# Performance work log

Hardware: AMD Instinct MI355X
Metric: run time of the kernel (lower is better)

The kernel has to match this reference:

```python
import jax, jax.numpy as jnp
import numpy as np

# ---- model constants (match init_kwargs) ----
N_USERS = 100_000
N_ITEMS = 50_000
N_ENTITIES = 200_000          # items are entities [0, N_ITEMS)
N_REL = 20                    # relations after the +1 shift; rel_weight has N_REL-1 rows
EMB = 64
HOPS = 2
MARGIN_CCL = 0.8
NUM_NEG = 64
ANGLE_W = 0.1
ANGLE_DROP = 0.5              # eval-mode Dropout(ones)*rate == constant rate scaling
N_EDGES = 1_000_000
NNZ = 1_000_000
N_TRIPLETS = 200_000
BATCH = 4096
EPS = 1e-6


def _l2norm(x):
    # torch F.normalize(dim=-1, eps=1e-12)
    return x / jnp.maximum(jnp.linalg.norm(x, axis=-1, keepdims=True), 1e-12)


def setup_inputs() -> dict:
    key = jax.random.key(0)
    ks = jax.random.split(key, 13)
    # xavier_uniform bounds: sqrt(6/(fan_in+fan_out))
    b_all = float(np.sqrt(6.0 / (N_USERS + N_ENTITIES + EMB)))
    b_cf = float(np.sqrt(6.0 / (N_ITEMS + EMB)))
    b_rel = float(np.sqrt(6.0 / (N_REL - 1 + EMB)))
    all_embed = jax.random.uniform(ks[0], (N_USERS + N_ENTITIES, EMB), jnp.float32, -b_all, b_all)
    item_emb_cf = jax.random.uniform(ks[1], (N_ITEMS, EMB), jnp.float32, -b_cf, b_cf)
    rel_weight = jax.random.uniform(ks[2], (N_REL - 1, EMB), jnp.float32, -b_rel, b_rel)
    # D^{-1/2} A row-normalized positive values
    interact_vals = jax.random.uniform(ks[3], (NNZ,), jnp.float32, 0.01, 0.3)
    user = jax.random.randint(ks[4], (BATCH,), 0, N_USERS)
    pos_item = jax.random.randint(ks[5], (BATCH,), 0, N_ITEMS)
    neg_item = jax.random.randint(ks[6], (BATCH, NUM_NEG), 0, N_ITEMS)
    edge_index = jax.random.randint(ks[7], (2, N_EDGES), 0, N_ENTITIES)
    edge_type = jax.random.randint(ks[8], (N_EDGES,), 1, N_REL)  # relations already +1 shifted
    interact_rows = jax.random.randint(ks[9], (NNZ,), 0, N_USERS)
    interact_cols = jax.random.randint(ks[10], (NNZ,), 0, N_ITEMS)  # URM cols live in item range
    triplet_h = jax.random.randint(ks[11], (N_TRIPLETS,), 0, N_ENTITIES)
    triplet_t = jax.random.randint(ks[12], (N_TRIPLETS,), 0, N_ITEMS)
    return dict(all_embed=all_embed, item_emb_cf=item_emb_cf, rel_weight=rel_weight,
                interact_vals=interact_vals, user=user, pos_item=pos_item, neg_item=neg_item,
                edge_index=edge_index, edge_type=edge_type, interact_rows=interact_rows,
                interact_cols=interact_cols, triplet_h=triplet_h, triplet_t=triplet_t)


def _gcn(user_emb, entity_emb, item_cf, rel_weight, edge_index, edge_type, rows, cols, vals):
    """Multi-hop HAKG GraphConv: relation-gated KG scatter-mean + sparse user/CF aggregation."""
    head, tail = edge_index[0], edge_index[1]
    ent_res, usr_res, cf_res = entity_emb, user_emb, item_cf
    cnt = jax.ops.segment_sum(jnp.ones(head.shape, entity_emb.dtype), head, N_ENTITIES)
    denom = jnp.maximum(cnt, 1.0)[:, None]            # scatter_mean denominator
    rel_e = rel_weight[edge_type - 1]                 # [E, D]
    for _ in range(HOPS):
        # KG aggregate: entity_agg[h] = mean_{(h,r,t)} entity[t] * rel[r]
        neigh = entity_emb[tail] * rel_e              # [E, D]
        entity_agg = jax.ops.segment_sum(neigh, head, N_ENTITIES) / denom
        # user aggregate: sparse interact_mat @ entity_emb
        user_agg = jax.ops.segment_sum(vals[:, None] * entity_emb[cols], rows, N_USERS)
        # CF branch (LightGCN-style): R @ item_cf then R^T @ (...)
        u_cf = jax.ops.segment_sum(vals[:, None] * item_cf[cols], rows, N_USERS)
        item_agg_cf = jax.ops.segment_sum(vals[:, None] * u_cf[rows], cols, N_ITEMS)
        entity_emb = _l2norm(entity_agg)
        user_emb = _l2norm(user_agg)
        item_cf = _l2norm(item_agg_cf)
        ent_res = ent_res + entity_emb
        usr_res = usr_res + user_emb
        cf_res = cf_res + item_cf
    return ent_res, usr_res, cf_res


def _half_aperture(u):
    K = 0.1
    sqnu = jnp.clip(jnp.sum(u * u, -1), 0.0, 1.0 - EPS)
    return jnp.arcsin(jnp.clip(K * (1.0 - sqnu) / jnp.sqrt(sqnu), -1.0 + EPS, 1.0 - EPS))


def _angle_at_u(u, v):
    nu = jnp.linalg.norm(u, axis=-1)
    nv = jnp.linalg.norm(v, axis=-1)
    dp = jnp.sum(u * v, -1)
    ed = jnp.linalg.norm(u - v, axis=-1)
    num = dp * (1.0 + nu ** 2) - nu ** 2 * (1.0 + nv ** 2)
    den = nu * ed * jnp.sqrt(jnp.clip(1.0 + nv ** 2 * nu ** 2 - 2.0 * dp, EPS, None)) + EPS
    return jnp.arccos(jnp.clip(num / den, -1.0 + EPS, 1.0 - EPS))


def _contrastive_loss(u_e, pos_e, neg_e, pos_cf, neg_cf):
    B = u_e.shape[0]
    u, p, n = _l2norm(u_e), _l2norm(pos_e), _l2norm(neg_e)
    pcf, ncf = _l2norm(pos_cf), _l2norm(neg_cf)
    ui_pos = jax.nn.relu(2.0 - (jnp.sum(u * p, -1) + jnp.sum(u * pcf, -1)))
    ub = jnp.repeat(u, NUM_NEG, axis=0)               # [B*K, D]
    def neg_loss(nn_):
        s = jax.nn.relu(jnp.sum(ub * nn_, -1) - MARGIN_CCL).reshape(B, NUM_NEG)
        return jnp.sum(s, -1) / (jnp.sum(s > 0, -1).astype(s.dtype) + 1e-5)
    return jnp.mean(ui_pos + neg_loss(n) + neg_loss(ncf))


def reference(all_embed, item_emb_cf, rel_weight, interact_vals, user, pos_item, neg_item,
              edge_index, edge_type, interact_rows, interact_cols, triplet_h, triplet_t):
    user_emb = all_embed[:N_USERS]
    entity_emb = all_embed[N_USERS:]
    ent_g, usr_g, cf_g = _gcn(user_emb, entity_emb, item_emb_cf, rel_weight,
                              edge_index, edge_type, interact_rows, interact_cols, interact_vals)
    flat_neg = neg_item.reshape(-1)
    u_e = usr_g[user]
    loss1 = _contrastive_loss(u_e, ent_g[pos_item], ent_g[flat_neg], cf_g[pos_item], cf_g[flat_neg])
    # angle (hierarchy) loss, vectorized over all cross-type triplets
    hs = entity_emb[triplet_h] * ANGLE_DROP
    ts = entity_emb[triplet_t] * ANGLE_DROP
    angle_half = jax.nn.relu(_angle_at_u(hs, ts) - _half_aperture(hs))
    loss2 = ANGLE_W * jnp.sum(angle_half) / N_TRIPLETS
    return loss1 + loss2
```

## Files before the change

kernel.cpp:

```cpp
#include <hip/hip_runtime.h>
#include <math.h>

#define N_USERS    100000
#define N_ITEMS    50000
#define N_ENTITIES 200000
#define N_REL      20
#define EMB        64
#define HOPS       2
#define MARGIN_CCL 0.8f
#define NUM_NEG    64
#define ANGLE_W    0.1f
#define ANGLE_DROP 0.5f
#define N_EDGES    1000000
#define NNZ        1000000
#define N_TRIPLETS 200000
#define BATCH      4096
#define EPSF       1e-6f

#define TILE1 2048
#define NBUCK 196
#define ACAP  8192
#define HBLK  ((N_EDGES + TILE1 - 1) / TILE1)
#define P1B   (3 * HBLK)
#define KGB   (N_ENTITIES / 32)
#define UCFB  (N_USERS / 32)
#define ITEMB ((N_ITEMS + 31) / 32)
#define UBB   (BATCH / 32)
#define ANGB  (N_TRIPLETS / 32)
#define LOSSB (BATCH / 4)
#define CONV4E (N_ENTITIES * 16 / 1024)
#define CONV4I ((N_ITEMS * 16 + 1023) / 1024)

typedef _Float16 half4_t __attribute__((ext_vector_type(4)));
typedef _Float16 half8_t __attribute__((ext_vector_type(8)));
typedef float float8_t __attribute__((ext_vector_type(8)));

__device__ inline float4 h2f(half4_t h) {
    return make_float4((float)h.x, (float)h.y, (float)h.z, (float)h.w);
}
__device__ inline half4_t f2h(float4 f) {
    half4_t h; h.x = (_Float16)f.x; h.y = (_Float16)f.y;
    h.z = (_Float16)f.z; h.w = (_Float16)f.w; return h;
}
__device__ inline float8_t h8_to_f8(half8_t h) { return __builtin_convertvector(h, float8_t); }
__device__ inline half8_t f8_to_h8(float8_t f) { return __builtin_convertvector(f, half8_t); }
__device__ inline half8_t h8_zero() {
    half8_t z;
    #pragma unroll
    for (int i = 0; i < 8; ++i) z[i] = (_Float16)0.0f;
    return z;
}
__device__ inline float sum_sq8(float8_t f) {
    float s = 0.f;
    #pragma unroll
    for (int i = 0; i < 8; ++i) s += f[i] * f[i];
    return s;
}
__device__ inline float dot8(float8_t a, float8_t b) {
    float s = 0.f;
    #pragma unroll
    for (int i = 0; i < 8; ++i) s += a[i] * b[i];
    return s;
}
__device__ inline float8_t f8_from2(float4 lo, float4 hi) {
    float8_t f;
    f[0] = lo.x; f[1] = lo.y; f[2] = lo.z; f[3] = lo.w;
    f[4] = hi.x; f[5] = hi.y; f[6] = hi.z; f[7] = hi.w;
    return f;
}
__device__ inline float grp_red8(float v) {
    v += __shfl_xor(v, 1, 64); v += __shfl_xor(v, 2, 64); v += __shfl_xor(v, 4, 64);
    return v;
}
__device__ inline float dot4(float4 a, float4 b) {
    return a.x * b.x + a.y * b.y + a.z * b.z + a.w * b.w;
}
__device__ inline float grp_red16(float v) {
    v += __shfl_xor(v, 1, 64); v += __shfl_xor(v, 2, 64);
    v += __shfl_xor(v, 4, 64); v += __shfl_xor(v, 8, 64);
    return v;
}
__device__ inline float cross_grp_scalar(float v) {
    v += __shfl_xor(v, 16, 64); v += __shfl_xor(v, 32, 64);
    return v;
}
__device__ inline int f32_to_h16bits(float v) {
    _Float16 h = (_Float16)v;
    return (int)__builtin_bit_cast(unsigned short, h);
}
__device__ inline _Float16 h16_from_bits(int b) {
    return __builtin_bit_cast(_Float16, (unsigned short)(b & 0xFFFF));
}

__device__ inline void angle_body(int ablk, int t, const half8_t* __restrict__ ent_h,
                                  const int* __restrict__ th, const int* __restrict__ tt,
                                  float* sb, float* __restrict__ l2blk) {
    int o = t & 7;
    int grp = t >> 3;
    int trip = ablk * 32 + grp;
    int h = th[trip], t2 = tt[trip];
    float8_t hv = h8_to_f8(ent_h[h * 8 + o]);
    float8_t tv = h8_to_f8(ent_h[t2 * 8 + o]);
    hv *= ANGLE_DROP;
    tv *= ANGLE_DROP;
    float8_t dv = hv - tv;
    float s_hh = grp_red8(sum_sq8(hv));
    float s_tt = grp_red8(sum_sq8(tv));
    float s_ht = grp_red8(dot8(hv, tv));
    float s_dd = grp_red8(sum_sq8(dv));
    if (o == 0) {
        float nu = sqrtf(s_hh);
        float ed = sqrtf(s_dd);
        float sqnu = fminf(fmaxf(s_hh, 0.0f), 1.0f - EPSF);
        float ha_arg = fminf(fmaxf(0.1f * (1.0f - sqnu) / sqrtf(sqnu), -1.0f + EPSF), 1.0f - EPSF);
        float half_ap = asinf(ha_arg);
        float num = s_ht * (1.0f + s_hh) - s_hh * (1.0f + s_tt);
        float den = nu * ed * sqrtf(fmaxf(1.0f + s_tt * s_hh - 2.0f * s_ht, EPSF)) + EPSF;
        float ang = acosf(fminf(fmaxf(num / den, -1.0f + EPSF), 1.0f - EPSF));
        sb[grp] = fmaxf(ang - half_ap, 0.0f);
    }
    __syncthreads();
    if (t == 0) {
        float tot = 0.f;
        #pragma unroll
        for (int i = 0; i < 32; ++i) tot += sb[i];
        l2blk[ablk] = tot;
    }
}

__global__ void __launch_bounds__(256) phase1_sort(
        const int* __restrict__ head, const int* __restrict__ tail,
        const int* __restrict__ etype, const int* __restrict__ rows,
        const int* __restrict__ cols, const float* __restrict__ vals,
        int* __restrict__ bcur_e, int* __restrict__ bcur_u, int* __restrict__ bcur_i,
        int* __restrict__ keys_ping, int* __restrict__ kg_ping,
        int2* __restrict__ u_ping, int2* __restrict__ i_ping,
        const float4* __restrict__ ent0, const float4* __restrict__ cf0,
        half4_t* __restrict__ ent_a4, half4_t* __restrict__ cf16a4) {
    __shared__ int2 pay_st[TILE1];
    __shared__ int lhist[256], lstart[256], lcur[256];
    __shared__ int wsum[4], wpre[4];
    int* gbase = lhist;
    int bx = blockIdx.x, t = threadIdx.x;
    if (bx >= P1B) {
        int cb = bx - P1B;
        if (cb < CONV4E) {
            int i = cb * 1024 + t;
            #pragma unroll
            for (int j = 0; j < 4; ++j) ent_a4[i + j * 256] = f2h(ent0[i + j * 256]);
        } else {
            int i = (cb - CONV4E) * 1024 + t;
            #pragma unroll
            for (int j = 0; j < 4; ++j) {
                int ii = i + j * 256;
                if (ii < N_ITEMS * 16) cf16a4[ii] = f2h(cf0[ii]);
            }
        }
        return;
    }
    int seg = bx / HBLK;
    int tb  = bx % HBLK;
    int tstart = tb * TILE1;
    int valid = min(TILE1, N_EDGES - tstart);
    const int* karr = (seg == 0) ? head : (seg == 1) ? rows : cols;
    int shift = (seg == 0) ? 10 : (seg == 1) ? 9 : 8;
    int* bcur = (seg == 0) ? bcur_e : (seg == 1) ? bcur_u : bcur_i;
    lhist[t] = 0;
    __syncthreads();
    int kreg[8], pxr[8], pyr[8];
    #pragma unroll
    for (int j = 0; j < 8; ++j) {
        int i = t + j * 256;
        if (i < valid) {
            int k = karr[tstart + i];
            kreg[j] = k;
            if (seg == 0) {
                pxr[j] = tail[tstart + i] | ((etype[tstart + i] - 1) << 18);
            } else {
                int px;
                if (seg == 1) px = cols[tstart + i] | ((k & 511) << 16);
                else          px = rows[tstart + i] | ((k & 255) << 17);
                pxr[j] = px;
                pyr[j] = f32_to_h16bits(vals[tstart + i]) | ((k >> shift) << 16);
            }
            atomicAdd(&lhist[k >> shift], 1);
        }
    }
    __syncthreads();
    int v = lhist[t];
    int lane = t & 63, wv = t >> 6;
    int sc = v;
    #pragma unroll
    for (int d = 1; d < 64; d <<= 1) {
        int x = __shfl_up(sc, d, 64);
        if (lane >= d) sc += x;
    }
    if (lane == 63) wsum[wv] = sc;
    __syncthreads();
    if (t == 0) {
        int a = 0;
        #pragma unroll
        for (int i = 0; i < 4; ++i) { wpre[i] = a; a += wsum[i]; }
    }
    __syncthreads();
    int excl = sc + wpre[wv] - v;
    lstart[t] = excl;
    lcur[t] = excl;
    gbase[t] = t * ACAP + atomicAdd(&bcur[t], v);
    __syncthreads();
    if (seg == 0) {
        int* key_st = (int*)pay_st;
        int* ps = key_st + TILE1;
        #pragma unroll
        for (int j = 0; j < 8; ++j) {
            int i = t + j * 256;
            if (i < valid) {
                int sp = atomicAdd(&lcur[kreg[j] >> 10], 1);
                key_st[sp] = kreg[j];
                ps[sp] = pxr[j];
            }
        }
        __syncthreads();
        for (int j = t; j < valid; j += 256) {
            int k = key_st[j];
            int b = k >> 10;
            int pos = gbase[b] + (j - lstart[b]);
            keys_ping[pos] = k;
            kg_ping[pos] = ps[j];
        }
    } else {
        int2* pay = (seg == 1) ? u_ping : i_ping;
        #pragma unroll
        for (int j = 0; j < 8; ++j) {
            int i = t + j * 256;
            if (i < valid) {
                int sp = atomicAdd(&lcur[kreg[j] >> shift], 1);
                pay_st[sp] = make_int2(pxr[j], pyr[j]);
            }
        }
        __syncthreads();
        for (int j = t; j < valid; j += 256) {
            int2 p = pay_st[j];
            int bb = (p.y >> 16) & 0xFF;
            int pos = gbase[bb] + (j - lstart[bb]);
            pay[pos] = p;
        }
    }
}

__global__ void __launch_bounds__(256) phase2_angle(
        const int* __restrict__ bcur_e, const int* __restrict__ keys_ping,
        const int* __restrict__ kg_ping, int* __restrict__ kg_pack, int* __restrict__ off_e,
        const int* __restrict__ bcur_u, const int2* __restrict__ u_ping,
        int2* __restrict__ u_pack, int* __restrict__ off_u,
        const int* __restrict__ bcur_i, const int2* __restrict__ i_ping,
        int2* __restrict__ i_pack, int* __restrict__ off_i,
        const half8_t* __restrict__ ent_a, const int* __restrict__ th,
        const int* __restrict__ tt, float* __restrict__ l2blk) {
    __shared__ int hist[1024];
    __shared__ int wsum[4], wpre[4];
    __shared__ float sb[32];
    int t = threadIdx.x;
    if (blockIdx.x >= 3 * NBUCK) {
        angle_body(blockIdx.x - 3 * NBUCK, t, ent_a, th, tt, sb, l2blk);
        return;
    }
    int seg = blockIdx.x / NBUCK;
    int b   = blockIdx.x % NBUCK;
    int bins  = (seg == 0) ? 1024 : (seg == 1) ? 512 : 256;
    int shift = (seg == 0) ? 10 : (seg == 1) ? 9 : 8;
    int n_rows = (seg == 0) ? N_ENTITIES : (seg == 1) ? N_USERS : N_ITEMS;
    const int* bcur = (seg == 0) ? bcur_e : (seg == 1) ? bcur_u : bcur_i;
    int* off = (seg == 0) ? off_e : (seg == 1) ? off_u : off_i;
    int rs = b << shift;
    int re = min(rs + bins, n_rows);
    int nr = re - rs;
    int base = b * ACAP;
    int len = bcur[b];
    for (int r = t; r < bins; r += 256) hist[r] = 0;
    __syncthreads();
    if (seg == 0) {
        for (int j = t; j < len; j += 256) atomicAdd(&hist[keys_ping[base + j] - rs], 1);
    } else if (seg == 1) {
        for (int j = t; j < len; j += 256) atomicAdd(&hist[(u_ping[base + j].x >> 16) & 511], 1);
    } else {
        for (int j = t; j < len; j += 256) atomicAdd(&hist[(i_ping[base + j].x >> 17) & 255], 1);
    }
    __syncthreads();
    int own = bins >> 8;
    int c[4]; int tot = 0;
    #pragma unroll
    for (int i = 0; i < 4; ++i) { c[i] = (i < own) ? hist[t * own + i] : 0; tot += c[i]; }
    int lane = t & 63, wv = t >> 6;
    int sc = tot;
    #pragma unroll
    for (int d = 1; d < 64; d <<= 1) {
        int x = __shfl_up(sc, d, 64);
        if (lane >= d) sc += x;
    }
    if (lane == 63) wsum[wv] = sc;
    __syncthreads();
    if (t == 0) {
        int a = 0;
        #pragma unroll
        for (int i = 0; i < 4; ++i) { wpre[i] = a; a += wsum[i]; }
    }
    __syncthreads();
    int run = sc + wpre[wv] - tot;
    #pragma unroll
    for (int i = 0; i < 4; ++i) { if (i < own) { hist[t * own + i] = run; run += c[i]; } }
    __syncthreads();
    for (int r = t; r < nr; r += 256) off[rs + b + r] = base + hist[r];
    if (t == 0) off[rs + b + nr] = base + len;
    __syncthreads();
    if (seg == 0) {
        for (int j = t; j < len; j += 256) {
            int k = keys_ping[base + j];
            int slot = atomicAdd(&hist[k - rs], 1);
            kg_pack[base + slot] = kg_ping[base + j];
        }
    } else if (seg == 1) {
        for (int j = t; j < len; j += 256) {
            int2 p = u_ping[base + j];
            int slot = atomicAdd(&hist[(p.x >> 16) & 511], 1);
            u_pack[base + slot] = p;
        }
    } else {
        for (int j = t; j < len; j += 256) {
            int2 p = i_ping[base + j];
            int slot = atomicAdd(&hist[(p.x >> 17) & 255], 1);
            i_pack[base + slot] = p;
        }
    }
}

__device__ inline void kg0_body(int bid, int t, const int* __restrict__ off,
                                const int* __restrict__ pack, half8_t* srel,
                                const float* __restrict__ relw,
                                const half8_t* __restrict__ src, half8_t* __restrict__ dst,
                                half8_t* __restrict__ res, const float4* __restrict__ res_init) {
    if (t < (N_REL - 1) * 8) {
        int rel = t >> 3, o = t & 7;
        const float4* r4 = (const float4*)relw;
        srel[rel * 9 + o] = f8_to_h8(f8_from2(r4[rel * 16 + o * 2], r4[rel * 16 + o * 2 + 1]));
    }
    __syncthreads();
    int row = bid * 32 + (t >> 3);
    int o = t & 7;
    int idx = row + (row >> 10);
    int s = off[idx], e = off[idx + 1];
    half8_t acc = h8_zero();
    int k = s;
    for (; k + 4 <= e; k += 4) {
        int p0 = pack[k], p1 = pack[k + 1], p2 = pack[k + 2], p3 = pack[k + 3];
        half8_t a0 = src[(p0 & 0x3FFFF) * 8 + o];
        half8_t a1 = src[(p1 & 0x3FFFF) * 8 + o];
        half8_t a2 = src[(p2 & 0x3FFFF) * 8 + o];
        half8_t a3 = src[(p3 & 0x3FFFF) * 8 + o];
        acc += a0 * srel[(p0 >> 18) * 9 + o];
        acc += a1 * srel[(p1 >> 18) * 9 + o];
        acc += a2 * srel[(p2 >> 18) * 9 + o];
        acc += a3 * srel[(p3 >> 18) * 9 + o];
    }
    for (; k < e; ++k) {
        int p0 = pack[k];
        acc += src[(p0 & 0x3FFFF) * 8 + o] * srel[(p0 >> 18) * 9 + o];
    }
    float8_t f = h8_to_f8(acc);
    f *= 1.0f / fmaxf((float)(e - s), 1.0f);
    float ss = grp_red8(sum_sq8(f));
    f *= 1.0f / fmaxf(sqrtf(ss), 1e-12f);
    dst[row * 8 + o] = f8_to_h8(f);
    if (row < N_ITEMS) {
        float8_t rr = f8_from2(res_init[row * 16 + o * 2], res_init[row * 16 + o * 2 + 1]);
        rr += f;
        res[row * 8 + o] = f8_to_h8(rr);
    }
}

__device__ inline void kg2_body(int bid, int t, const int* __restrict__ off,
                                const int* __restrict__ pack, half8_t* srel,
                                const float* __restrict__ relw,
                                const half8_t* __restrict__ src, half8_t* __restrict__ res) {
    if (t < (N_REL - 1) * 8) {
        int rel = t >> 3, o = t & 7;
        const float4* r4 = (const float4*)relw;
        srel[rel * 9 + o] = f8_to_h8(f8_from2(r4[rel * 16 + o * 2], r4[rel * 16 + o * 2 + 1]));
    }
    __syncthreads();
    int row = bid * 32 + (t >> 3);
    if (row >= N_ITEMS) return;
    int o = t & 7;
    int idx = row + (row >> 10);
    int s = off[idx], e = off[idx + 1];
    half8_t acc = h8_zero();
    int k = s;
    for (; k + 4 <= e; k += 4) {
        int p0 = pack[k], p1 = pack[k + 1], p2 = pack[k + 2], p3 = pack[k + 3];
        half8_t a0 = src[(p0 & 0x3FFFF) * 8 + o];
        half8_t a1 = src[(p1 & 0x3FFFF) * 8 + o];
        half8_t a2 = src[(p2 & 0x3FFFF) * 8 + o];
        half8_t a3 = src[(p3 & 0x3FFFF) * 8 + o];
        acc += a0 * srel[(p0 >> 18) * 9 + o];
        acc += a1 * srel[(p1 >> 18) * 9 + o];
        acc += a2 * srel[(p2 >> 18) * 9 + o];
        acc += a3 * srel[(p3 >> 18) * 9 + o];
    }
    for (; k < e; ++k) {
        int p0 = pack[k];
        acc += src[(p0 & 0x3FFFF) * 8 + o] * srel[(p0 >> 18) * 9 + o];
    }
    float8_t f = h8_to_f8(acc);
    f *= 1.0f / fmaxf((float)(e - s), 1.0f);
    float ss = grp_red8(sum_sq8(f));
    f *= 1.0f / fmaxf(sqrtf(ss), 1e-12f);
    float8_t rr = h8_to_f8(res[row * 8 + o]);
    rr += f;
    float s2 = grp_red8(sum_sq8(rr));
    rr *= 1.0f / fmaxf(sqrtf(s2), 1e-12f);
    res[row * 8 + o] = f8_to_h8(rr);
}

__device__ inline void ucf_body(int bid, int t, const int* __restrict__ off,
                                const int2* __restrict__ u_pack,
                                const half8_t* __restrict__ cf16,
                                half8_t* __restrict__ ucf) {
    int row = bid * 32 + (t >> 3);
    int o = t & 7;
    int idx = row + (row >> 9);
    int s = off[idx], e = off[idx + 1];
    half8_t acc = h8_zero();
    int k = s;
    if (k + 4 <= e) {
        int2 p0 = u_pack[k], p1 = u_pack[k + 1], p2 = u_pack[k + 2], p3 = u_pack[k + 3];
        for (;;) {
            int kn = k + 4;
            half8_t c0 = cf16[(p0.x & 0xFFFF) * 8 + o];
            half8_t c1 = cf16[(p1.x & 0xFFFF) * 8 + o];
            half8_t c2 = cf16[(p2.x & 0xFFFF) * 8 + o];
            half8_t c3 = cf16[(p3.x & 0xFFFF) * 8 + o];
            bool more = (kn + 4 <= e);
            int2 n0, n1, n2, n3;
            if (more) { n0 = u_pack[kn]; n1 = u_pack[kn + 1]; n2 = u_pack[kn + 2]; n3 = u_pack[kn + 3]; }
            acc += c0 * h16_from_bits(p0.y);
            acc += c1 * h16_from_bits(p1.y);
            acc += c2 * h16_from_bits(p2.y);
            acc += c3 * h16_from_bits(p3.y);
            k = kn;
            if (!more) break;
            p0 = n0; p1 = n1; p2 = n2; p3 = n3;
        }
    }
    for (; k < e; ++k) {
        int2 p0 = u_pack[k];
        acc += cf16[(p0.x & 0xFFFF) * 8 + o] * h16_from_bits(p0.y);
    }
    ucf[row * 8 + o] = acc;
}

__device__ inline void ubatch_body(int bid, int t, const int* __restrict__ user,
                                   const int* __restrict__ off,
                                   const int2* __restrict__ u_pack,
                                   const half8_t* __restrict__ ent_a,
                                   const half8_t* __restrict__ ent_b,
                                   const float4* __restrict__ usr0f,
                                   half8_t* __restrict__ usr_b) {
    int g = t >> 3, o = t & 7;
    int b = bid * 32 + g;
    int uid = user[b];
    int idx = uid + (uid >> 9);
    int s = off[idx], e = off[idx + 1];
    half8_t acc1 = h8_zero(), acc2 = h8_zero();
    int k = s;
    for (; k + 4 <= e; k += 4) {
        int2 p0 = u_pack[k], p1 = u_pack[k + 1], p2 = u_pack[k + 2], p3 = u_pack[k + 3];
        int c0 = (p0.x & 0xFFFF) * 8 + o;
        int c1 = (p1.x & 0xFFFF) * 8 + o;
        int c2 = (p2.x & 0xFFFF) * 8 + o;
        int c3 = (p3.x & 0xFFFF) * 8 + o;
        half8_t ea0 = ent_a[c0], eb0 = ent_b[c0];
        half8_t ea1 = ent_a[c1], eb1 = ent_b[c1];
        half8_t ea2 = ent_a[c2], eb2 = ent_b[c2];
        half8_t ea3 = ent_a[c3], eb3 = ent_b[c3];
        _Float16 v0 = h16_from_bits(p0.y);
        _Float16 v1 = h16_from_bits(p1.y);
        _Float16 v2 = h16_from_bits(p2.y);
        _Float16 v3 = h16_from_bits(p3.y);
        acc1 += ea0 * v0; acc2 += eb0 * v0;
        acc1 += ea1 * v1; acc2 += eb1 * v1;
        acc1 += ea2 * v2; acc2 += eb2 * v2;
        acc1 += ea3 * v3; acc2 += eb3 * v3;
    }
    for (; k < e; ++k) {
        int2 p0 = u_pack[k];
        int c0 = (p0.x & 0xFFFF) * 8 + o;
        _Float16 v0 = h16_from_bits(p0.y);
        acc1 += ent_a[c0] * v0;
        acc2 += ent_b[c0] * v0;
    }
    float8_t f1 = h8_to_f8(acc1);
    float ss1 = grp_red8(sum_sq8(f1));
    f1 *= 1.0f / fmaxf(sqrtf(ss1), 1e-12f);
    float8_t u0 = f8_from2(usr0f[uid * 16 + o * 2], usr0f[uid * 16 + o * 2 + 1]);
    float8_t r1 = h8_to_f8(f8_to_h8(u0 + f1));
    float8_t f2 = h8_to_f8(acc2);
    float ss2 = grp_red8(sum_sq8(f2));
    f2 *= 1.0f / fmaxf(sqrtf(ss2), 1e-12f);
    float8_t r = r1 + f2;
    float s3 = grp_red8(sum_sq8(r));
    r *= 1.0f / fmaxf(sqrtf(s3), 1e-12f);
    usr_b[b * 8 + o] = f8_to_h8(r);
}

__device__ inline void item_body(int bid, int t, const int* __restrict__ off,
                                 const int2* __restrict__ i_pack,
                                 const half8_t* __restrict__ ucf,
                                 half8_t* __restrict__ cf_nxt, half8_t* __restrict__ res,
                                 const float4* __restrict__ res_init, int first, int last) {
    int row = bid * 32 + (t >> 3);
    int o = t & 7;
    if (row >= N_ITEMS) return;
    int idx = row + (row >> 8);
    int s = off[idx], e = off[idx + 1];
    half8_t acc = h8_zero();
    int k = s;
    if (k + 4 <= e) {
        int2 p0 = i_pack[k], p1 = i_pack[k + 1], p2 = i_pack[k + 2], p3 = i_pack[k + 3];
        for (;;) {
            int kn = k + 4;
            half8_t c0 = ucf[(p0.x & 0x1FFFF) * 8 + o];
            half8_t c1 = ucf[(p1.x & 0x1FFFF) * 8 + o];
            half8_t c2 = ucf[(p2.x & 0x1FFFF) * 8 + o];
            half8_t c3 = ucf[(p3.x & 0x1FFFF) * 8 + o];
            bool more = (kn + 4 <= e);
            int2 n0, n1, n2, n3;
            if (more) { n0 = i_pack[kn]; n1 = i_pack[kn + 1]; n2 = i_pack[kn + 2]; n3 = i_pack[kn + 3]; }
            acc += c0 * h16_from_bits(p0.y);
            acc += c1 * h16_from_bits(p1.y);
            acc += c2 * h16_from_bits(p2.y);
            acc += c3 * h16_from_bits(p3.y);
            k = kn;
            if (!more) break;
            p0 = n0; p1 = n1; p2 = n2; p3 = n3;
        }
    }
    for (; k < e; ++k) {
        int2 p0 = i_pack[k];
        acc += ucf[(p0.x & 0x1FFFF) * 8 + o] * h16_from_bits(p0.y);
    }
    float8_t f = h8_to_f8(acc);
    float ss = grp_red8(sum_sq8(f));
    f *= 1.0f / fmaxf(sqrtf(ss), 1e-12f);
    if (!last) cf_nxt[row * 8 + o] = f8_to_h8(f);
    float8_t rr;
    if (first) rr = f8_from2(res_init[row * 16 + o * 2], res_init[row * 16 + o * 2 + 1]);
    else       rr = h8_to_f8(res[row * 8 + o]);
    rr += f;
    if (last) {
        float s2 = grp_red8(sum_sq8(rr));
        rr *= 1.0f / fmaxf(sqrtf(s2), 1e-12f);
    }
    res[row * 8 + o] = f8_to_h8(rr);
}

__device__ inline void loss_ent_body(int b, int t,
                                     const int* __restrict__ pos, const int* __restrict__ neg,
                                     const half4_t* __restrict__ usrb4,
                                     const half4_t* __restrict__ ent4,
                                     float* __restrict__ dpe, float* __restrict__ l1pe) {
    int lane = t & 63;
    int g = lane >> 4, q = lane & 15;
    int pid = pos[b];
    float4 u = h2f(usrb4[b * 16 + q]);
    float4 p = h2f(ent4[pid * 16 + q]);
    float dpe_v = grp_red16(dot4(u, p));
    float sum_n = 0.f, cnt_n = 0.f;
    const int* nb = neg + b * NUM_NEG;
    for (int j = 0; j < NUM_NEG; j += 16) {
        int n0 = nb[j + g], n1 = nb[j + 4 + g], n2 = nb[j + 8 + g], n3 = nb[j + 12 + g];
        float4 e0 = h2f(ent4[n0 * 16 + q]);
        float4 e1 = h2f(ent4[n1 * 16 + q]);
        float4 e2 = h2f(ent4[n2 * 16 + q]);
        float4 e3 = h2f(ent4[n3 * 16 + q]);
        float dn0 = grp_red16(dot4(u, e0));
        float dn1 = grp_red16(dot4(u, e1));
        float dn2 = grp_red16(dot4(u, e2));
        float dn3 = grp_red16(dot4(u, e3));
        float s0 = fmaxf(dn0 - MARGIN_CCL, 0.f); sum_n += s0; if (s0 > 0.f) cnt_n += 1.f;
        float s1 = fmaxf(dn1 - MARGIN_CCL, 0.f); sum_n += s1; if (s1 > 0.f) cnt_n += 1.f;
        float s2 = fmaxf(dn2 - MARGIN_CCL, 0.f); sum_n += s2; if (s2 > 0.f) cnt_n += 1.f;
        float s3 = fmaxf(dn3 - MARGIN_CCL, 0.f); sum_n += s3; if (s3 > 0.f) cnt_n += 1.f;
    }
    sum_n = cross_grp_scalar(sum_n); cnt_n = cross_grp_scalar(cnt_n);
    if (lane == 0) {
        dpe[b] = dpe_v;
        l1pe[b] = sum_n / (cnt_n + 1e-5f);
    }
}

__global__ void __launch_bounds__(256) loss_cf_kernel(
        const int* __restrict__ pos, const int* __restrict__ neg,
        const half4_t* __restrict__ usrb4, const half4_t* __restrict__ cf4,
        const float* __restrict__ dpe, const float* __restrict__ l1pe,
        float* __restrict__ l1p) {
    int b = blockIdx.x * 4 + (threadIdx.x >> 6);
    int lane = threadIdx.x & 63;
    int g = lane >> 4, q = lane & 15;
    int pid = pos[b];
    float4 u = h2f(usrb4[b * 16 + q]);
    float4 pc = h2f(cf4[pid * 16 + q]);
    float dpc = grp_red16(dot4(u, pc));
    float sum_c = 0.f, cnt_c = 0.f;
    const int* nb = neg + b * NUM_NEG;
    for (int j = 0; j < NUM_NEG; j += 16) {
        int n0 = nb[j + g], n1 = nb[j + 4 + g], n2 = nb[j + 8 + g], n3 = nb[j + 12 + g];
        float4 e0 = h2f(cf4[n0 * 16 + q]);
        float4 e1 = h2f(cf4[n1 * 16 + q]);
        float4 e2 = h2f(cf4[n2 * 16 + q]);
        float4 e3 = h2f(cf4[n3 * 16 + q]);
        float dc0 = grp_red16(dot4(u, e0));
        float dc1 = grp_red16(dot4(u, e1));
        float dc2 = grp_red16(dot4(u, e2));
        float dc3 = grp_red16(dot4(u, e3));
        float t0 = fmaxf(dc0 - MARGIN_CCL, 0.f); sum_c += t0; if (t0 > 0.f) cnt_c += 1.f;
        float t1 = fmaxf(dc1 - MARGIN_CCL, 0.f); sum_c += t1; if (t1 > 0.f) cnt_c += 1.f;
        float t2 = fmaxf(dc2 - MARGIN_CCL, 0.f); sum_c += t2; if (t2 > 0.f) cnt_c += 1.f;
        float t3 = fmaxf(dc3 - MARGIN_CCL, 0.f); sum_c += t3; if (t3 > 0.f) cnt_c += 1.f;
    }
    sum_c = cross_grp_scalar(sum_c); cnt_c = cross_grp_scalar(cnt_c);
    if (lane == 0) {
        float ui_pos = fmaxf(2.0f - dpe[b] - dpc, 0.0f);
        l1p[b] = ui_pos + l1pe[b] + sum_c / (cnt_c + 1e-5f);
    }
}

__global__ void __launch_bounds__(256) fused_h0(
        const int* __restrict__ off_e, const int* __restrict__ kg_pack,
        const float* __restrict__ relw, const half8_t* __restrict__ ent_a,
        half8_t* __restrict__ ent_b, half8_t* __restrict__ ent_res,
        const float4* __restrict__ ent0f,
        const int* __restrict__ off_u, const int2* __restrict__ u_pack,
        const half8_t* __restrict__ cf16_a, half8_t* __restrict__ ucf) {
    __shared__ half8_t srel[(N_REL - 1) * 9];
    int bx = blockIdx.x, t = threadIdx.x;
    if (bx < KGB) {
        kg0_body(bx, t, off_e, kg_pack, srel, relw, ent_a, ent_b, ent_res, ent0f);
    } else {
        ucf_body(bx - KGB, t, off_u, u_pack, cf16_a, ucf);
    }
}

__global__ void __launch_bounds__(256) fused_ik(
        const int* __restrict__ off_e, const int* __restrict__ kg_pack,
        const float* __restrict__ relw, const half8_t* __restrict__ ent_b,
        half8_t* __restrict__ ent_res,
        const int* __restrict__ off_i, const int2* __restrict__ i_pack,
        const half8_t* __restrict__ ucf, half8_t* __restrict__ cf16_b,
        half8_t* __restrict__ cf_res, const float4* __restrict__ cf0f,
        const int* __restrict__ user, const int* __restrict__ off_u,
        const int2* __restrict__ u_pack, const half8_t* __restrict__ ent_a,
        const float4* __restrict__ usr0f, half8_t* __restrict__ usr_b) {
    __shared__ half8_t srel[(N_REL - 1) * 9];
    int bx = blockIdx.x, t = threadIdx.x;
    if (bx < ITEMB) {
        kg2_body(bx, t, off_e, kg_pack, srel, relw, ent_b, ent_res);
    } else if (bx < 2 * ITEMB) {
        item_body(bx - ITEMB, t, off_i, i_pack, ucf, cf16_b, cf_res, cf0f, 1, 0);
    } else {
        ubatch_body(bx - 2 * ITEMB, t, user, off_u, u_pack, ent_a, ent_b, usr0f, usr_b);
    }
}

__global__ void __launch_bounds__(256) fused_u1_loss(
        const int* __restrict__ off_u, const int2* __restrict__ u_pack,
        const half8_t* __restrict__ cf16_b, half8_t* __restrict__ ucf,
        const int* __restrict__ pos, const int* __restrict__ neg,
        const half4_t* __restrict__ usrb4, const half4_t* __restrict__ ent4,
        float* __restrict__ dpe, float* __restrict__ l1pe) {
    int bx = blockIdx.x, t = threadIdx.x;
    if (bx < UCFB) {
        ucf_body(bx, t, off_u, u_pack, cf16_b, ucf);
    } else {
        int b = (bx - UCFB) * 4 + (t >> 6);
        loss_ent_body(b, t, pos, neg, usrb4, ent4, dpe, l1pe);
    }
}

__global__ void __launch_bounds__(256) item_h1(
        const int* __restrict__ off_i, const int2* __restrict__ i_pack,
        const half8_t* __restrict__ ucf, half8_t* __restrict__ cf_res,
        const float4* __restrict__ cf0f) {
    item_body(blockIdx.x, threadIdx.x, off_i, i_pack, ucf, (half8_t*)0, cf_res, cf0f, 0, 1);
}

__global__ void finalize_kernel(const float* __restrict__ l1p, const float* __restrict__ l2b,
                                float* __restrict__ out) {
    __shared__ float sb[1024];
    float a1 = 0.f;
    for (int i = threadIdx.x; i < BATCH; i += 1024) a1 += l1p[i];
    float a2 = 0.f;
    for (int i = threadIdx.x; i < ANGB; i += 1024) a2 += l2b[i];
    sb[threadIdx.x] = a1 / (float)BATCH + ANGLE_W * a2 / (float)N_TRIPLETS;
    __syncthreads();
    for (int s = 512; s > 0; s >>= 1) {
        if (threadIdx.x < s) sb[threadIdx.x] += sb[threadIdx.x + s];
        __syncthreads();
    }
    if (threadIdx.x == 0) out[0] = sb[0];
}

extern "C" void kernel_launch(void* const* d_in, const int* in_sizes, int n_in,
                              void* d_out, int out_size, void* d_ws, size_t ws_size,
                              hipStream_t stream) {
    const float* all_embed = (const float*)d_in[0];
    const float* item_cf0  = (const float*)d_in[1];
    const float* relw      = (const float*)d_in[2];
    const float* vals      = (const float*)d_in[3];
    const int* user        = (const int*)d_in[4];
    const int* pos_item    = (const int*)d_in[5];
    const int* neg_item    = (const int*)d_in[6];
    const int* edge_head   = (const int*)d_in[7];
    const int* edge_tail   = edge_head + N_EDGES;
    const int* etype       = (const int*)d_in[8];
    const int* irows       = (const int*)d_in[9];
    const int* icols       = (const int*)d_in[10];
    const int* th          = (const int*)d_in[11];
    const int* tt          = (const int*)d_in[12];
    float* out             = (float*)d_out;

    char* base = (char*)d_ws;
    size_t woff = 0;
    auto alloc = [&](size_t bytes) -> void* {
        void* p = base + woff;
        woff = (woff + bytes + 255) & ~(size_t)255;
        return p;
    };
    const size_t ping_ui = (size_t)NBUCK * ACAP * 8;
    const size_t ping_kg = (size_t)NBUCK * ACAP * 4;

    half8_t* ent_a   = (half8_t*)alloc((size_t)N_ENTITIES * EMB * 2);
    half8_t* ent_b   = (half8_t*)alloc(2 * ping_ui);
    half8_t* cf16_a  = (half8_t*)alloc((size_t)N_ITEMS * EMB * 2);
    half8_t* cf16_b  = (half8_t*)alloc(ping_kg);
    half8_t* ucf     = (half8_t*)alloc((size_t)N_USERS * EMB * 2);
    half8_t* ent_res = (half8_t*)alloc((size_t)N_ITEMS * EMB * 2);
    half8_t* cf_res  = (half8_t*)alloc((size_t)N_ITEMS * EMB * 2);
    half8_t* usr_b   = (half8_t*)alloc((size_t)BATCH * EMB * 2);
    int2* u_pack     = (int2*)alloc(ping_ui);
    int2* i_pack     = (int2*)alloc(ping_ui);
    int* kg_pack     = (int*)alloc(ping_kg);
    float* l1p       = (float*)alloc((size_t)BATCH * 4);
    float* dpe       = (float*)alloc((size_t)BATCH * 4);
    float* l1pe      = (float*)alloc((size_t)BATCH * 4);
    float* l2blk     = (float*)alloc((size_t)ANGB * 4);
    int* off_e       = (int*)alloc((size_t)(N_ENTITIES + NBUCK + 1) * 4);
    int* off_u       = (int*)alloc((size_t)(N_USERS + NBUCK + 1) * 4);
    int* off_i       = (int*)alloc((size_t)(N_ITEMS + NBUCK + 1) * 4);
    int* bcur_all    = (int*)alloc(3 * 256 * 4);
    int* bcur_e      = bcur_all;
    int* bcur_u      = bcur_all + 256;
    int* bcur_i      = bcur_all + 512;

    int2* u_ping   = (int2*)ent_b;
    int2* i_ping   = (int2*)((char*)ent_b + ping_ui);
    int* kg_ping   = (int*)cf16_b;
    int* keys_ping = (int*)ucf;

    const float* ent0 = all_embed + (size_t)N_USERS * EMB;

    hipMemsetAsync(bcur_all, 0, 3 * 256 * 4, stream);
    phase1_sort<<<P1B + CONV4E + CONV4I, 256, 0, stream>>>(
        edge_head, edge_tail, etype, irows, icols, vals,
        bcur_e, bcur_u, bcur_i, keys_ping, kg_ping, u_ping, i_ping,
        (const float4*)ent0, (const float4*)item_cf0, (half4_t*)ent_a, (half4_t*)cf16_a);
    phase2_angle<<<3 * NBUCK + ANGB, 256, 0, stream>>>(
        bcur_e, keys_ping, kg_ping, kg_pack, off_e,
        bcur_u, u_ping, u_pack, off_u,
        bcur_i, i_ping, i_pack, off_i,
        (const half8_t*)ent_a, th, tt, l2blk);
    fused_h0<<<KGB + UCFB, 256, 0, stream>>>(
        off_e, kg_pack, relw, ent_a, ent_b, ent_res, (const float4*)ent0,
        off_u, u_pack, cf16_a, ucf);
    fused_ik<<<2 * ITEMB + UBB, 256, 0, stream>>>(
        off_e, kg_pack, relw, ent_b, ent_res,
        off_i, i_pack, ucf, cf16_b, cf_res, (const float4*)item_cf0,
        user, off_u, u_pack, ent_a, (const float4*)all_embed, usr_b);
    fused_u1_loss<<<UCFB + LOSSB, 256, 0, stream>>>(
        off_u, u_pack, cf16_b, ucf, pos_item, neg_item,
        (const half4_t*)usr_b, (const half4_t*)ent_res, dpe, l1pe);
    item_h1<<<ITEMB, 256, 0, stream>>>(off_i, i_pack, ucf, cf_res,
                                       (const float4*)item_cf0);
    loss_cf_kernel<<<LOSSB, 256, 0, stream>>>(pos_item, neg_item,
                                              (const half4_t*)usr_b, (const half4_t*)cf_res,
                                              dpe, l1pe, l1p);
    finalize_kernel<<<1, 1024, 0, stream>>>(l1p, l2blk, out);
}
```

Baseline: 343.8 us.

## Spread angle-loss blocks across later kernels and prefetch gather indices

The angle-loss blocks are split three ways. Part stays in phase2, and the rest are appended to the item_h1 and loss_cf kernels, which have small grids, so the tail of each launch gets filled with independent work. Separately, the KG aggregation loops and the negative-sample loss loops now software-pipeline their index loads, fetching the next group of indices while the current gathers are used. This adds register pressure and makes block scheduling in those kernels mixed, and it relies on ent_a still holding valid data at the later launches.

```diff
diff --git a/kernel.cpp b/kernel.cpp
--- a/kernel.cpp
+++ b/kernel.cpp
@@ -30,6 +30,9 @@
 #define LOSSB (BATCH / 4)
 #define CONV4E (N_ENTITIES * 16 / 1024)
 #define CONV4I ((N_ITEMS * 16 + 1023) / 1024)
+#define ANG_P2 2048
+#define ANG_IT 2101
+#define ANG_LC (ANGB - ANG_P2 - ANG_IT)
 
 typedef _Float16 half4_t __attribute__((ext_vector_type(4)));
 typedef _Float16 half8_t __attribute__((ext_vector_type(8)));
@@ -351,16 +354,25 @@
     int s = off[idx], e = off[idx + 1];
     half8_t acc = h8_zero();
     int k = s;
-    for (; k + 4 <= e; k += 4) {
+    if (k + 4 <= e) {
         int p0 = pack[k], p1 = pack[k + 1], p2 = pack[k + 2], p3 = pack[k + 3];
-        half8_t a0 = src[(p0 & 0x3FFFF) * 8 + o];
-        half8_t a1 = src[(p1 & 0x3FFFF) * 8 + o];
-        half8_t a2 = src[(p2 & 0x3FFFF) * 8 + o];
-        half8_t a3 = src[(p3 & 0x3FFFF) * 8 + o];
-        acc += a0 * srel[(p0 >> 18) * 9 + o];
-        acc += a1 * srel[(p1 >> 18) * 9 + o];
-        acc += a2 * srel[(p2 >> 18) * 9 + o];
-        acc += a3 * srel[(p3 >> 18) * 9 + o];
+        for (;;) {
+            int kn = k + 4;
+            half8_t a0 = src[(p0 & 0x3FFFF) * 8 + o];
+            half8_t a1 = src[(p1 & 0x3FFFF) * 8 + o];
+            half8_t a2 = src[(p2 & 0x3FFFF) * 8 + o];
+            half8_t a3 = src[(p3 & 0x3FFFF) * 8 + o];
+            bool more = (kn + 4 <= e);
+            int q0, q1, q2, q3;
+            if (more) { q0 = pack[kn]; q1 = pack[kn + 1]; q2 = pack[kn + 2]; q3 = pack[kn + 3]; }
+            acc += a0 * srel[(p0 >> 18) * 9 + o];
+            acc += a1 * srel[(p1 >> 18) * 9 + o];
+            acc += a2 * srel[(p2 >> 18) * 9 + o];
+            acc += a3 * srel[(p3 >> 18) * 9 + o];
+            k = kn;
+            if (!more) break;
+            p0 = q0; p1 = q1; p2 = q2; p3 = q3;
+        }
     }
     for (; k < e; ++k) {
         int p0 = pack[k];
@@ -395,16 +407,25 @@
     int s = off[idx], e = off[idx + 1];
     half8_t acc = h8_zero();
     int k = s;
-    for (; k + 4 <= e; k += 4) {
+    if (k + 4 <= e) {
         int p0 = pack[k], p1 = pack[k + 1], p2 = pack[k + 2], p3 = pack[k + 3];
-        half8_t a0 = src[(p0 & 0x3FFFF) * 8 + o];
-        half8_t a1 = src[(p1 & 0x3FFFF) * 8 + o];
-        half8_t a2 = src[(p2 & 0x3FFFF) * 8 + o];
-        half8_t a3 = src[(p3 & 0x3FFFF) * 8 + o];
-        acc += a0 * srel[(p0 >> 18) * 9 + o];
-        acc += a1 * srel[(p1 >> 18) * 9 + o];
-        acc += a2 * srel[(p2 >> 18) * 9 + o];
-        acc += a3 * srel[(p3 >> 18) * 9 + o];
+        for (;;) {
+            int kn = k + 4;
+            half8_t a0 = src[(p0 & 0x3FFFF) * 8 + o];
+            half8_t a1 = src[(p1 & 0x3FFFF) * 8 + o];
+            half8_t a2 = src[(p2 & 0x3FFFF) * 8 + o];
+            half8_t a3 = src[(p3 & 0x3FFFF) * 8 + o];
+            bool more = (kn + 4 <= e);
+            int q0, q1, q2, q3;
+            if (more) { q0 = pack[kn]; q1 = pack[kn + 1]; q2 = pack[kn + 2]; q3 = pack[kn + 3]; }
+            acc += a0 * srel[(p0 >> 18) * 9 + o];
+            acc += a1 * srel[(p1 >> 18) * 9 + o];
+            acc += a2 * srel[(p2 >> 18) * 9 + o];
+            acc += a3 * srel[(p3 >> 18) * 9 + o];
+            k = kn;
+            if (!more) break;
+            p0 = q0; p1 = q1; p2 = q2; p3 = q3;
+        }
     }
     for (; k < e; ++k) {
         int p0 = pack[k];
@@ -576,12 +597,18 @@
     float dpe_v = grp_red16(dot4(u, p));
     float sum_n = 0.f, cnt_n = 0.f;
     const int* nb = neg + b * NUM_NEG;
+    int n0 = nb[g], n1 = nb[4 + g], n2 = nb[8 + g], n3 = nb[12 + g];
     for (int j = 0; j < NUM_NEG; j += 16) {
-        int n0 = nb[j + g], n1 = nb[j + 4 + g], n2 = nb[j + 8 + g], n3 = nb[j + 12 + g];
         float4 e0 = h2f(ent4[n0 * 16 + q]);
         float4 e1 = h2f(ent4[n1 * 16 + q]);
         float4 e2 = h2f(ent4[n2 * 16 + q]);
         float4 e3 = h2f(ent4[n3 * 16 + q]);
+        bool more = (j + 16 < NUM_NEG);
+        int m0, m1, m2, m3;
+        if (more) {
+            m0 = nb[j + 16 + g]; m1 = nb[j + 20 + g];
+            m2 = nb[j + 24 + g]; m3 = nb[j + 28 + g];
+        }
         float dn0 = grp_red16(dot4(u, e0));
         float dn1 = grp_red16(dot4(u, e1));
         float dn2 = grp_red16(dot4(u, e2));
@@ -590,6 +617,7 @@
         float s1 = fmaxf(dn1 - MARGIN_CCL, 0.f); sum_n += s1; if (s1 > 0.f) cnt_n += 1.f;
         float s2 = fmaxf(dn2 - MARGIN_CCL, 0.f); sum_n += s2; if (s2 > 0.f) cnt_n += 1.f;
         float s3 = fmaxf(dn3 - MARGIN_CCL, 0.f); sum_n += s3; if (s3 > 0.f) cnt_n += 1.f;
+        if (more) { n0 = m0; n1 = m1; n2 = m2; n3 = m3; }
     }
     sum_n = cross_grp_scalar(sum_n); cnt_n = cross_grp_scalar(cnt_n);
     if (lane == 0) {
@@ -602,7 +630,14 @@
         const int* __restrict__ pos, const int* __restrict__ neg,
         const half4_t* __restrict__ usrb4, const half4_t* __restrict__ cf4,
         const float* __restrict__ dpe, const float* __restrict__ l1pe,
-        float* __restrict__ l1p) {
+        float* __restrict__ l1p,
+        const half8_t* __restrict__ ent_a, const int* __restrict__ th,
+        const int* __restrict__ tt, float* __restrict__ l2blk) {
+    __shared__ float sb[32];
+    if (blockIdx.x >= LOSSB) {
+        angle_body(ANG_P2 + ANG_IT + (blockIdx.x - LOSSB), threadIdx.x, ent_a, th, tt, sb, l2blk);
+        return;
+    }
     int b = blockIdx.x * 4 + (threadIdx.x >> 6);
     int lane = threadIdx.x & 63;
     int g = lane >> 4, q = lane & 15;
@@ -612,12 +647,18 @@
     float dpc = grp_red16(dot4(u, pc));
     float sum_c = 0.f, cnt_c = 0.f;
     const int* nb = neg + b * NUM_NEG;
+    int n0 = nb[g], n1 = nb[4 + g], n2 = nb[8 + g], n3 = nb[12 + g];
     for (int j = 0; j < NUM_NEG; j += 16) {
-        int n0 = nb[j + g], n1 = nb[j + 4 + g], n2 = nb[j + 8 + g], n3 = nb[j + 12 + g];
         float4 e0 = h2f(cf4[n0 * 16 + q]);
         float4 e1 = h2f(cf4[n1 * 16 + q]);
         float4 e2 = h2f(cf4[n2 * 16 + q]);
         float4 e3 = h2f(cf4[n3 * 16 + q]);
+        bool more = (j + 16 < NUM_NEG);
+        int m0, m1, m2, m3;
+        if (more) {
+            m0 = nb[j + 16 + g]; m1 = nb[j + 20 + g];
+            m2 = nb[j + 24 + g]; m3 = nb[j + 28 + g];
+        }
         float dc0 = grp_red16(dot4(u, e0));
         float dc1 = grp_red16(dot4(u, e1));
         float dc2 = grp_red16(dot4(u, e2));
@@ -626,6 +667,7 @@
         float t1 = fmaxf(dc1 - MARGIN_CCL, 0.f); sum_c += t1; if (t1 > 0.f) cnt_c += 1.f;
         float t2 = fmaxf(dc2 - MARGIN_CCL, 0.f); sum_c += t2; if (t2 > 0.f) cnt_c += 1.f;
         float t3 = fmaxf(dc3 - MARGIN_CCL, 0.f); sum_c += t3; if (t3 > 0.f) cnt_c += 1.f;
+        if (more) { n0 = m0; n1 = m1; n2 = m2; n3 = m3; }
     }
     sum_c = cross_grp_scalar(sum_c); cnt_c = cross_grp_scalar(cnt_c);
     if (lane == 0) {
@@ -689,7 +731,14 @@
 __global__ void __launch_bounds__(256) item_h1(
         const int* __restrict__ off_i, const int2* __restrict__ i_pack,
         const half8_t* __restrict__ ucf, half8_t* __restrict__ cf_res,
-        const float4* __restrict__ cf0f) {
+        const float4* __restrict__ cf0f,
+        const half8_t* __restrict__ ent_a, const int* __restrict__ th,
+        const int* __restrict__ tt, float* __restrict__ l2blk) {
+    __shared__ float sb[32];
+    if (blockIdx.x >= ITEMB) {
+        angle_body(ANG_P2 + (blockIdx.x - ITEMB), threadIdx.x, ent_a, th, tt, sb, l2blk);
+        return;
+    }
     item_body(blockIdx.x, threadIdx.x, off_i, i_pack, ucf, (half8_t*)0, cf_res, cf0f, 0, 1);
 }
 
@@ -773,7 +822,7 @@
         edge_head, edge_tail, etype, irows, icols, vals,
         bcur_e, bcur_u, bcur_i, keys_ping, kg_ping, u_ping, i_ping,
         (const float4*)ent0, (const float4*)item_cf0, (half4_t*)ent_a, (half4_t*)cf16_a);
-    phase2_angle<<<3 * NBUCK + ANGB, 256, 0, stream>>>(
+    phase2_angle<<<3 * NBUCK + ANG_P2, 256, 0, stream>>>(
         bcur_e, keys_ping, kg_ping, kg_pack, off_e,
         bcur_u, u_ping, u_pack, off_u,
         bcur_i, i_ping, i_pack, off_i,
@@ -788,10 +837,12 @@
     fused_u1_loss<<<UCFB + LOSSB, 256, 0, stream>>>(
         off_u, u_pack, cf16_b, ucf, pos_item, neg_item,
         (const half4_t*)usr_b, (const half4_t*)ent_res, dpe, l1pe);
-    item_h1<<<ITEMB, 256, 0, stream>>>(off_i, i_pack, ucf, cf_res,
-                                       (const float4*)item_cf0);
-    loss_cf_kernel<<<LOSSB, 256, 0, stream>>>(pos_item, neg_item,
-                                              (const half4_t*)usr_b, (const half4_t*)cf_res,
-                                              dpe, l1pe, l1p);
+    item_h1<<<ITEMB + ANG_IT, 256, 0, stream>>>(off_i, i_pack, ucf, cf_res,
+                                                (const float4*)item_cf0,
+                                                (const half8_t*)ent_a, th, tt, l2blk);
+    loss_cf_kernel<<<LOSSB + ANG_LC, 256, 0, stream>>>(pos_item, neg_item,
+                                                       (const half4_t*)usr_b, (const half4_t*)cf_res,
+                                                       dpe, l1pe, l1p,
+                                                       (const half8_t*)ent_a, th, tt, l2blk);
     finalize_kernel<<<1, 1024, 0, stream>>>(l1p, l2blk, out);
 }
```

After: 346.6 us. Within noise of the previous version (+0.8%).
